# Kernel optimization log

Hardware: AMD Instinct MI355X
Metric: run time of the kernel (lower is better)

The kernel has to match this reference:

```python
import jax, jax.numpy as jnp
import numpy as np

B, T, V, E, H, C, L = 32, 120, 32000, 256, 512, 20, 10
LN_EPS = 1e-5

# static span enumeration matching the original loop order:
# for begin in range(T): for span_len in 1..L if begin+span_len-1 < T
_begs, _lens = [], []
for _b in range(T):
    for _l in range(1, min(L, T - _b) + 1):
        _begs.append(_b); _lens.append(_l)
BEGS = np.asarray(_begs, np.int32)   # [S], S = 1155
LENS = np.asarray(_lens, np.int32)
S = len(_begs)


def setup_inputs() -> dict:
    key = jax.random.key(0)
    ks = jax.random.split(key, 12)
    rn = lambda k, shape, s=0.05: (jax.random.normal(k, shape, jnp.float32) * s)
    return {
        "tokens": jax.random.randint(ks[0], (B, T), 0, V, dtype=jnp.int32),
        "emb": rn(ks[1], (V, E)),
        "w_ih_f": rn(ks[2], (4 * H, E)), "w_hh_f": rn(ks[3], (4 * H, H)),
        "b_ih_f": jnp.zeros((4 * H,), jnp.float32), "b_hh_f": jnp.zeros((4 * H,), jnp.float32),
        "w_ih_b": rn(ks[4], (4 * H, E)), "w_hh_b": rn(ks[5], (4 * H, H)),
        "b_ih_b": jnp.zeros((4 * H,), jnp.float32), "b_hh_b": jnp.zeros((4 * H,), jnp.float32),
        "lin1_w": rn(ks[6], (H, 2 * H)), "lin1_b": jnp.zeros((H,), jnp.float32),
        "lin2_w": rn(ks[7], (H, H)), "lin2_b": jnp.zeros((H,), jnp.float32),
        "ln_g": jnp.ones((H,), jnp.float32), "ln_b": jnp.zeros((H,), jnp.float32),
        "label_w": rn(ks[8], (H, C)), "label_b": rn(ks[9], (C,)),
    }


def _lstm_dir(x, w_ih, w_hh, b_ih, b_hh, reverse):
    # x: [B, T, E] -> hs: [B, T, H]; torch gate order i, f, g, o
    xs = jnp.swapaxes(x, 0, 1)          # [T, B, E]
    if reverse:
        xs = xs[::-1]
    xg = xs @ w_ih.T + (b_ih + b_hh)    # [T, B, 4H] input contribution precomputed
    h0 = jnp.zeros((x.shape[0], w_hh.shape[1]), x.dtype)

    def step(carry, g_in):
        h, c = carry
        g = g_in + h @ w_hh.T
        i, f, gg, o = jnp.split(g, 4, axis=-1)
        c = jax.nn.sigmoid(f) * c + jax.nn.sigmoid(i) * jnp.tanh(gg)
        h = jax.nn.sigmoid(o) * jnp.tanh(c)
        return (h, c), h

    _, hs = jax.lax.scan(step, (h0, h0), xg)
    if reverse:
        hs = hs[::-1]
    return jnp.swapaxes(hs, 0, 1)


def reference(tokens, emb, w_ih_f, w_hh_f, b_ih_f, b_hh_f,
              w_ih_b, w_hh_b, b_ih_b, b_hh_b,
              lin1_w, lin1_b, lin2_w, lin2_b, ln_g, ln_b,
              label_w, label_b):
    x = emb[tokens]                                          # [B, T, E]
    fwd = _lstm_dir(x, w_ih_f, w_hh_f, b_ih_f, b_hh_f, False)
    bwd = _lstm_dir(x, w_ih_b, w_hh_b, b_ih_b, b_hh_b, True)
    rnn_out = jnp.concatenate([fwd, bwd], axis=-1)           # [B, T, 2H]

    # non_linear: Linear -> Dropout(eval: identity) -> ReLU -> Linear -> LayerNorm
    h = jax.nn.relu(rnn_out @ lin1_w.T + lin1_b)
    h = h @ lin2_w.T + lin2_b
    mu = jnp.mean(h, axis=-1, keepdims=True)
    var = jnp.var(h, axis=-1, keepdims=True)
    token_repr = (h - mu) / jnp.sqrt(var + LN_EPS) * ln_g + ln_b  # [B, T, H]

    # span mean pooling via exclusive cumsum: mean over [beg, beg+len)
    cs = jnp.concatenate(
        [jnp.zeros_like(token_repr[:, :1]), jnp.cumsum(token_repr, axis=1)], axis=1)  # [B, T+1, H]
    begs = jnp.asarray(BEGS)
    ends = jnp.asarray(BEGS + LENS)
    inv_len = 1.0 / jnp.asarray(LENS, token_repr.dtype)[:, None]
    spans = (cs[:, ends] - cs[:, begs]) * inv_len            # [B, S, H]
    span_reprs = spans.reshape(-1, spans.shape[-1])          # [B*S, H], bid-major order

    score = jax.nn.log_softmax(span_reprs @ label_w + label_b, axis=0)
    return score
```

## Files before the change

kernel.cpp:

```cpp
#include <hip/hip_runtime.h>

#define B_ 32
#define T_ 120
#define E_ 256
#define H_ 512
#define NSPAN 36960

typedef __attribute__((ext_vector_type(8))) short short8;
typedef __attribute__((ext_vector_type(4))) short sshort4;
typedef __attribute__((ext_vector_type(4))) float f32x4;
typedef __attribute__((ext_vector_type(4))) unsigned int u32x4;
typedef unsigned long long ull;

__device__ __forceinline__ short f2bf(float x) {
    union { float f; unsigned u; } v; v.f = x;
    unsigned r = v.u + 0x7fffu + ((v.u >> 16) & 1u);
    return (short)(r >> 16);
}
__device__ __forceinline__ float bf2f(unsigned short x) {
    union { unsigned u; float f; } v; v.u = ((unsigned)x) << 16;
    return v.f;
}

#define LDC(dst, addr) \
    asm volatile("global_load_dwordx4 %0, %1, off sc0 sc1" : "=v"(dst) : "v"(addr))

__global__ void k_gather(const int* __restrict__ tokens, const float* __restrict__ emb,
                         short* __restrict__ xbf) {
    int m = blockIdx.x;
    int t = m >> 5, b = m & 31;
    int tok = tokens[b * T_ + t];
    int e = threadIdx.x;
    xbf[(size_t)m * E_ + e] = f2bf(emb[(size_t)tok * E_ + e]);
}

__global__ void k_convert(const float* __restrict__ src, short* __restrict__ dst, int n8) {
    int i = blockIdx.x * blockDim.x + threadIdx.x;
    if (i >= n8) return;
    const float4* s4 = (const float4*)src + (size_t)i * 2;
    float4 a = s4[0], b = s4[1];
    short8 o;
    o[0]=f2bf(a.x); o[1]=f2bf(a.y); o[2]=f2bf(a.z); o[3]=f2bf(a.w);
    o[4]=f2bf(b.x); o[5]=f2bf(b.y); o[6]=f2bf(b.z); o[7]=f2bf(b.w);
    *(short8*)(dst + (size_t)i * 8) = o;
}

__global__ void k_biascomb(const float* __restrict__ bf1, const float* __restrict__ bf2,
                           const float* __restrict__ bb1, const float* __restrict__ bb2,
                           float* __restrict__ out) {
    int i = blockIdx.x * 256 + threadIdx.x;
    out[i] = (i < 2048) ? (bf1[i] + bf2[i]) : (bb1[i - 2048] + bb2[i - 2048]);
}

template <int EPI>
__global__ void __launch_bounds__(256) k_gemm(const short* __restrict__ A,
                                              const short* __restrict__ W,
                                              const float* __restrict__ bias,
                                              float* __restrict__ outF,
                                              short* __restrict__ outB,
                                              int N, int K) {
    int w = threadIdx.x >> 6, l = threadIdx.x & 63;
    int la = l & 15, lb = l >> 4;
    int m0 = blockIdx.x * 64 + w * 16;
    int nb = blockIdx.y * 64;
    const short* Ap = A + (size_t)(m0 + la) * K + lb * 8;
    const short* Wp = W + (size_t)(nb + la) * K + lb * 8;
    f32x4 acc0 = {0.f,0.f,0.f,0.f}, acc1 = acc0, acc2 = acc0, acc3 = acc0;
    for (int k0 = 0; k0 < K; k0 += 32) {
        short8 a  = *(const short8*)(Ap + k0);
        short8 b0 = *(const short8*)(Wp + k0);
        short8 b1 = *(const short8*)(Wp + (size_t)16 * K + k0);
        short8 b2 = *(const short8*)(Wp + (size_t)32 * K + k0);
        short8 b3 = *(const short8*)(Wp + (size_t)48 * K + k0);
        acc0 = __builtin_amdgcn_mfma_f32_16x16x32_bf16(a, b0, acc0, 0, 0, 0);
        acc1 = __builtin_amdgcn_mfma_f32_16x16x32_bf16(a, b1, acc1, 0, 0, 0);
        acc2 = __builtin_amdgcn_mfma_f32_16x16x32_bf16(a, b2, acc2, 0, 0, 0);
        acc3 = __builtin_amdgcn_mfma_f32_16x16x32_bf16(a, b3, acc3, 0, 0, 0);
    }
    f32x4 accs[4] = {acc0, acc1, acc2, acc3};
    #pragma unroll
    for (int j = 0; j < 4; ++j) {
        int n = nb + j * 16 + la;
        float bv = bias[n];
        if (EPI == 2) {
            int mb = m0 + lb * 4;
            int t = mb >> 5, b0i = mb & 31;
            sshort4 pk;
            #pragma unroll
            for (int r = 0; r < 4; ++r) pk[r] = f2bf(accs[j][r] + bv);
            *(sshort4*)(outB + (((size_t)t * 4096 + n) << 5) + b0i) = pk;
        } else {
            #pragma unroll
            for (int r = 0; r < 4; ++r) {
                int m = m0 + lb * 4 + r;
                float v = accs[j][r] + bv;
                if (EPI == 0) outF[(size_t)m * N + n] = v;
                else          outB[(size_t)m * N + n] = f2bf(fmaxf(v, 0.f));
            }
        }
    }
}

__global__ void __launch_bounds__(256, 1) k_lstm(const short* __restrict__ xg,
                                                 const short* __restrict__ whh,
                                                 const short* __restrict__ hzero,
                                                 short* __restrict__ hsteps,
                                                 short* __restrict__ rnn) {
    __shared__ short wlds[4][16][512];
    __shared__ short hlds[32][512];
    __shared__ short hpack[4][32][4];
    int tid = threadIdx.x;
    int w = tid >> 6, l = tid & 63;
    int la = l & 15, lb = l >> 4;
    int bid = blockIdx.x;
    int dir = bid >> 5, jsl = bid & 31;
    int jw = jsl * 16 + w * 4;

    {
        char* base = (char*)&wlds[w][0][0];
        for (int cc = l; cc < 1024; cc += 64) {
            int rr = cc >> 6, c16 = cc & 63;
            int gate = rr >> 2, jj = rr & 3;
            short8 v = *(const short8*)(whh + ((size_t)dir * 2048 + gate * 512 + jw + jj) * 512 + c16 * 8);
            *(short8*)(base + rr * 1024 + ((c16 * 16) ^ ((rr & 7) << 4))) = v;
        }
    }
    __syncthreads();

    float cst[2][4] = {{0.f,0.f,0.f,0.f},{0.f,0.f,0.f,0.f}};
    int gate = la >> 2;
    int grow = dir * 2048 + gate * 512 + jw + (la & 3);
    const char* wrow = (const char*)&wlds[w][0][0] + la * 1024;
    const char* hrow0 = (const char*)&hlds[0][0] + la * 1024;
    const char* hrow1 = hrow0 + 16 * 1024;
    int swz = (la & 7) << 4;

    for (int s = 0; s < T_; ++s) {
        int t = dir ? (T_ - 1 - s) : s;
        const short* hb = (s == 0) ? hzero
                                   : (hsteps + ((size_t)(dir * T_ + (s - 1)) << 14));
        short* hn = hsteps + ((size_t)(dir * T_ + s) << 14);

        ull x0, x1;
        {
            u32x4 vv[8];
            const char* src = (const char*)hb;
            #pragma unroll
            for (int i = 0; i < 8; ++i)
                LDC(vv[i], src + (tid + 256 * i) * 16);
            const short* xgp = xg + ((size_t)t * 4096 + grow) * 32;
            x0 = *(const ull*)(xgp + lb * 4);
            x1 = *(const ull*)(xgp + 16 + lb * 4);
            asm volatile("s_waitcnt vmcnt(0)" ::: "memory");
            __builtin_amdgcn_sched_barrier(0);
            int tries = 0;
            while (true) {
                unsigned bad = 0;
                #pragma unroll
                for (int i = 0; i < 8; ++i)
                    if (vv[i][0] == 0xFFFFFFFFu || vv[i][2] == 0xFFFFFFFFu) bad |= 1u << i;
                if (!__any(bad != 0)) break;
                if (++tries > (1 << 17)) break;
                #pragma unroll
                for (int i = 0; i < 8; ++i)
                    if (bad & (1u << i)) LDC(vv[i], src + (tid + 256 * i) * 16);
                asm volatile("s_waitcnt vmcnt(0)" ::: "memory");
                __builtin_amdgcn_sched_barrier(0);
            }
            char* hdst = (char*)&hlds[0][0];
            #pragma unroll
            for (int i = 0; i < 8; ++i) {
                int byte = (tid + 256 * i) << 4;
                int row = byte >> 10, col = byte & 1023;
                *(u32x4*)(hdst + row * 1024 + (col ^ ((row & 7) << 4))) = vv[i];
            }
        }
        __syncthreads();

        float xv[2][4];
        #pragma unroll
        for (int r = 0; r < 4; ++r) {
            xv[0][r] = bf2f((unsigned short)((x0 >> (16 * r)) & 0xffffu));
            xv[1][r] = bf2f((unsigned short)((x1 >> (16 * r)) & 0xffffu));
        }

        f32x4 a0A = {0.f,0.f,0.f,0.f}, a0B = a0A, a1A = a0A, a1B = a0A;
        #pragma unroll
        for (int ks2 = 0; ks2 < 8; ++ks2) {
            int co0 = ((ks2 * 128) + lb * 16) ^ swz;
            int co1 = co0 ^ 64;
            short8 wA = *(const short8*)(wrow + co0);
            short8 wB = *(const short8*)(wrow + co1);
            short8 h0A = *(const short8*)(hrow0 + co0);
            short8 h0B = *(const short8*)(hrow0 + co1);
            short8 h1A = *(const short8*)(hrow1 + co0);
            short8 h1B = *(const short8*)(hrow1 + co1);
            a0A = __builtin_amdgcn_mfma_f32_16x16x32_bf16(h0A, wA, a0A, 0, 0, 0);
            a1A = __builtin_amdgcn_mfma_f32_16x16x32_bf16(h1A, wA, a1A, 0, 0, 0);
            a0B = __builtin_amdgcn_mfma_f32_16x16x32_bf16(h0B, wB, a0B, 0, 0, 0);
            a1B = __builtin_amdgcn_mfma_f32_16x16x32_bf16(h1B, wB, a1B, 0, 0, 0);
        }
        __syncthreads();
        f32x4 a0 = a0A + a0B, a1 = a1A + a1B;

        float val[2][4];
        #pragma unroll
        for (int mt = 0; mt < 2; ++mt) {
            #pragma unroll
            for (int r = 0; r < 4; ++r) {
                float x = (mt ? a1[r] : a0[r]) + xv[mt][r];
                val[mt][r] = (gate == 2) ? (1.f - 2.f / (1.f + __expf(2.f * x)))
                                         : (1.f / (1.f + __expf(-x)));
            }
        }

        #pragma unroll
        for (int mt = 0; mt < 2; ++mt) {
            #pragma unroll
            for (int r = 0; r < 4; ++r) {
                float v = val[mt][r];
                float vf = __shfl_xor(v, 4);
                float vg = __shfl_xor(v, 8);
                float vo = __shfl_xor(v, 12);
                if (la < 4) {
                    float c = vf * cst[mt][r] + v * vg;
                    cst[mt][r] = c;
                    float h = vo * (1.f - 2.f / (1.f + __expf(2.f * c)));
                    hpack[w][mt * 16 + lb * 4 + r][la] = f2bf(h);
                }
            }
        }
        asm volatile("s_waitcnt lgkmcnt(0)" ::: "memory");
        __builtin_amdgcn_sched_barrier(0);
        __builtin_amdgcn_wave_barrier();

        if (l < 32) {
            ull pk = *(const ull*)&hpack[w][l][0];
            short* hp = hn + (size_t)l * 512 + jw;
            asm volatile("global_store_dwordx2 %0, %1, off sc0 sc1" :: "v"(hp), "v"(pk) : "memory");
            *(ull*)(rnn + ((size_t)l * T_ + t) * 1024 + dir * 512 + jw) = pk;
        }
        __builtin_amdgcn_wave_barrier();
    }
}

__global__ void k_ln(const float* __restrict__ h2, const float* __restrict__ gam,
                     const float* __restrict__ bet, float* __restrict__ tr) {
    int w = threadIdx.x >> 6, l = threadIdx.x & 63;
    size_t row = (size_t)blockIdx.x * 4 + w;
    const float* x = h2 + row * 512;
    float v[8], s = 0.f, s2 = 0.f;
    #pragma unroll
    for (int i = 0; i < 8; ++i) { v[i] = x[l + 64 * i]; s += v[i]; s2 += v[i] * v[i]; }
    #pragma unroll
    for (int off = 32; off; off >>= 1) { s += __shfl_xor(s, off); s2 += __shfl_xor(s2, off); }
    float mu = s * (1.f / 512.f);
    float var = s2 * (1.f / 512.f) - mu * mu;
    float rstd = 1.f / sqrtf(var + 1e-5f);
    float* o = tr + row * 512;
    #pragma unroll
    for (int i = 0; i < 8; ++i) { int k = l + 64 * i; o[k] = (v[i] - mu) * rstd * gam[k] + bet[k]; }
}

__global__ void k_cumsum(const float* __restrict__ tr, float* __restrict__ cs) {
    int b = blockIdx.x, f = threadIdx.x;
    cs[((size_t)b * 121) * 512 + f] = 0.f;
    const float* src = tr + ((size_t)b * 120) * 512 + f;
    float* dst = cs + ((size_t)b * 121 + 1) * 512 + f;
    float run = 0.f;
    for (int t0 = 0; t0 < 120; t0 += 8) {
        float v[8];
        #pragma unroll
        for (int i = 0; i < 8; ++i) v[i] = src[(size_t)(t0 + i) * 512];
        #pragma unroll
        for (int i = 0; i < 8; ++i) { run += v[i]; dst[(size_t)(t0 + i) * 512] = run; }
    }
}

__global__ void __launch_bounds__(256) k_span(const float* __restrict__ cs,
                                              const float* __restrict__ lw,
                                              const float* __restrict__ lbias,
                                              float* __restrict__ out) {
    __shared__ float wl[20][512];
    for (int idx = threadIdx.x; idx < 20 * 512; idx += 256) {
        int c = idx >> 9, k = idx & 511;
        wl[c][k] = lw[(size_t)k * 20 + c];
    }
    __syncthreads();
    int w = threadIdx.x >> 6, l = threadIdx.x & 63;
    int nw = gridDim.x * 4;
    for (int sp = blockIdx.x * 4 + w; sp < NSPAN; sp += nw) {
        int b = sp / 1155, s = sp - b * 1155;
        int beg, len;
        if (s < 1110) { beg = s / 10; len = s - beg * 10 + 1; }
        else {
            int t2 = s - 1110; beg = 111; int ll = 9;
            while (t2 >= ll) { t2 -= ll; --ll; ++beg; }
            len = t2 + 1;
        }
        int end = beg + len;
        const float* ce = cs + ((size_t)b * 121 + end) * 512;
        const float* cb = cs + ((size_t)b * 121 + beg) * 512;
        float inv = 1.f / (float)len;
        float p[20];
        #pragma unroll
        for (int c = 0; c < 20; ++c) p[c] = 0.f;
        #pragma unroll
        for (int i = 0; i < 8; ++i) {
            int k = l + 64 * i;
            float d = (ce[k] - cb[k]) * inv;
            #pragma unroll
            for (int c = 0; c < 20; ++c) p[c] += d * wl[c][k];
        }
        #pragma unroll
        for (int off = 32; off; off >>= 1) {
            #pragma unroll
            for (int c = 0; c < 20; ++c) p[c] += __shfl_xor(p[c], off);
        }
        if (l == 0) {
            float* o = out + (size_t)sp * 20;
            #pragma unroll
            for (int c = 0; c < 20; ++c) o[c] = p[c] + lbias[c];
        }
    }
}

__global__ void __launch_bounds__(256) k_lsepart(const float* __restrict__ logits,
                                                 float2* __restrict__ part) {
    float m[20], sm[20];
    #pragma unroll
    for (int c = 0; c < 20; ++c) { m[c] = -1e30f; sm[c] = 0.f; }
    for (int row = blockIdx.x * 256 + threadIdx.x; row < NSPAN; row += gridDim.x * 256) {
        const float* r = logits + (size_t)row * 20;
        #pragma unroll
        for (int c = 0; c < 20; ++c) {
            float x = r[c];
            float nm = fmaxf(m[c], x);
            sm[c] = sm[c] * expf(m[c] - nm) + expf(x - nm);
            m[c] = nm;
        }
    }
    __shared__ float2 red[256][20];
    #pragma unroll
    for (int c = 0; c < 20; ++c) red[threadIdx.x][c] = make_float2(m[c], sm[c]);
    __syncthreads();
    for (int st = 128; st; st >>= 1) {
        if (threadIdx.x < st) {
            #pragma unroll
            for (int c = 0; c < 20; ++c) {
                float2 a = red[threadIdx.x][c], b = red[threadIdx.x + st][c];
                float nm = fmaxf(a.x, b.x);
                float ss = a.y * expf(a.x - nm) + b.y * expf(b.x - nm);
                red[threadIdx.x][c] = make_float2(nm, ss);
            }
        }
        __syncthreads();
    }
    if (threadIdx.x < 20) part[(size_t)blockIdx.x * 20 + threadIdx.x] = red[0][threadIdx.x];
}

__global__ void k_lsefin(const float2* __restrict__ part, int nparts, float* __restrict__ lse) {
    int c = threadIdx.x;
    if (c >= 20) return;
    float m = -1e30f, s = 0.f;
    for (int i = 0; i < nparts; ++i) {
        float2 a = part[(size_t)i * 20 + c];
        float nm = fmaxf(m, a.x);
        s = s * expf(m - nm) + a.y * expf(a.x - nm);
        m = nm;
    }
    lse[c] = m + logf(s);
}

__global__ void k_sub(float* __restrict__ out, const float* __restrict__ lse) {
    int i = blockIdx.x * 256 + threadIdx.x;
    if (i < NSPAN * 20) out[i] -= lse[i % 20];
}

extern "C" void kernel_launch(void* const* d_in, const int* in_sizes, int n_in,
                              void* d_out, int out_size, void* d_ws, size_t ws_size,
                              hipStream_t stream) {
    (void)in_sizes; (void)n_in; (void)out_size; (void)ws_size;
    const int*   tokens = (const int*)  d_in[0];
    const float* emb    = (const float*)d_in[1];
    const float* w_ih_f = (const float*)d_in[2];
    const float* w_hh_f = (const float*)d_in[3];
    const float* b_ih_f = (const float*)d_in[4];
    const float* b_hh_f = (const float*)d_in[5];
    const float* w_ih_b = (const float*)d_in[6];
    const float* w_hh_b = (const float*)d_in[7];
    const float* b_ih_b = (const float*)d_in[8];
    const float* b_hh_b = (const float*)d_in[9];
    const float* lin1_w = (const float*)d_in[10];
    const float* lin1_b = (const float*)d_in[11];
    const float* lin2_w = (const float*)d_in[12];
    const float* lin2_b = (const float*)d_in[13];
    const float* ln_g   = (const float*)d_in[14];
    const float* ln_b   = (const float*)d_in[15];
    const float* label_w= (const float*)d_in[16];
    const float* label_b= (const float*)d_in[17];
    float* out = (float*)d_out;

    char* ws = (char*)d_ws;
    size_t off = 0;
    auto alloc = [&](size_t bytes) { char* p = ws + off; off += (bytes + 255) & ~size_t(255); return p; };
    short*  xbf   = (short*)alloc(3840ull * 256 * 2);
    short*  wihbf = (short*)alloc(4096ull * 256 * 2);
    short*  whhbf = (short*)alloc(2ull * 2048 * 512 * 2);
    short*  l1wbf = (short*)alloc(512ull * 1024 * 2);
    short*  l2wbf = (short*)alloc(512ull * 512 * 2);
    float*  biasc = (float*)alloc(4096ull * 4);
    short*  xg    = (short*)alloc(120ull * 4096 * 32 * 2);
    short*  hzero = (short*)alloc(32ull * 512 * 2);
    short*  hsteps= (short*)alloc(2ull * 120 * 32 * 512 * 2);
    short*  rnn   = (short*)alloc(3840ull * 1024 * 2);
    float2* part  = (float2*)alloc(120ull * 20 * 8);
    float*  lse   = (float*)alloc(256);
    short*  h1    = (short*)whhbf;
    float*  h2    = (float*)hsteps;
    float*  tr    = (float*)xg;
    float*  cs    = (float*)((char*)xg + 8ull * 1024 * 1024);

    hipMemsetAsync(hzero, 0x00, 32ull * 512 * 2, stream);
    hipMemsetAsync(hsteps, 0xFF, 2ull * 120 * 32 * 512 * 2, stream);

    k_gather<<<3840, 256, 0, stream>>>(tokens, emb, xbf);
    int n8;
    n8 = 2048 * 256 / 8; k_convert<<<(n8 + 255) / 256, 256, 0, stream>>>(w_ih_f, wihbf, n8);
    n8 = 2048 * 256 / 8; k_convert<<<(n8 + 255) / 256, 256, 0, stream>>>(w_ih_b, wihbf + 2048ull * 256, n8);
    n8 = 2048 * 512 / 8; k_convert<<<(n8 + 255) / 256, 256, 0, stream>>>(w_hh_f, whhbf, n8);
    n8 = 2048 * 512 / 8; k_convert<<<(n8 + 255) / 256, 256, 0, stream>>>(w_hh_b, whhbf + 2048ull * 512, n8);
    n8 = 512 * 1024 / 8; k_convert<<<(n8 + 255) / 256, 256, 0, stream>>>(lin1_w, l1wbf, n8);
    n8 = 512 * 512 / 8;  k_convert<<<(n8 + 255) / 256, 256, 0, stream>>>(lin2_w, l2wbf, n8);
    k_biascomb<<<16, 256, 0, stream>>>(b_ih_f, b_hh_f, b_ih_b, b_hh_b, biasc);

    k_gemm<2><<<dim3(60, 64), 256, 0, stream>>>(xbf, wihbf, biasc, nullptr, xg, 4096, 256);
    k_lstm<<<64, 256, 0, stream>>>(xg, whhbf, hzero, hsteps, rnn);
    k_gemm<1><<<dim3(60, 8), 256, 0, stream>>>(rnn, l1wbf, lin1_b, nullptr, h1, 512, 1024);
    k_gemm<0><<<dim3(60, 8), 256, 0, stream>>>(h1, l2wbf, lin2_b, h2, nullptr, 512, 512);
    k_ln<<<960, 256, 0, stream>>>(h2, ln_g, ln_b, tr);
    k_cumsum<<<32, 512, 0, stream>>>(tr, cs);
    k_span<<<512, 256, 0, stream>>>(cs, label_w, label_b, out);
    k_lsepart<<<120, 256, 0, stream>>>(out, part);
    k_lsefin<<<1, 32, 0, stream>>>(part, 120, lse);
    k_sub<<<(NSPAN * 20 + 255) / 256, 256, 0, stream>>>(out, lse);
}
```

Baseline: 937.4 us.

## Keep LSTM weights in registers, add step counters, project before span pooling

After: 1.184 ms. 1.26x slower.

```diff
diff --git a/kernel.cpp b/kernel.cpp
--- a/kernel.cpp
+++ b/kernel.cpp
@@ -105,8 +105,8 @@
                                                  const short* __restrict__ whh,
                                                  const short* __restrict__ hzero,
                                                  short* __restrict__ hsteps,
-                                                 short* __restrict__ rnn) {
-    __shared__ short wlds[4][16][512];
+                                                 short* __restrict__ rnn,
+                                                 int* __restrict__ ctr) {
     __shared__ short hlds[32][512];
     __shared__ short hpack[4][32][4];
     int tid = threadIdx.x;
@@ -115,25 +115,22 @@
     int bid = blockIdx.x;
     int dir = bid >> 5, jsl = bid & 31;
     int jw = jsl * 16 + w * 4;
-
-    {
-        char* base = (char*)&wlds[w][0][0];
-        for (int cc = l; cc < 1024; cc += 64) {
-            int rr = cc >> 6, c16 = cc & 63;
-            int gate = rr >> 2, jj = rr & 3;
-            short8 v = *(const short8*)(whh + ((size_t)dir * 2048 + gate * 512 + jw + jj) * 512 + c16 * 8);
-            *(short8*)(base + rr * 1024 + ((c16 * 16) ^ ((rr & 7) << 4))) = v;
-        }
-    }
-    __syncthreads();
-
-    float cst[2][4] = {{0.f,0.f,0.f,0.f},{0.f,0.f,0.f,0.f}};
     int gate = la >> 2;
     int grow = dir * 2048 + gate * 512 + jw + (la & 3);
-    const char* wrow = (const char*)&wlds[w][0][0] + la * 1024;
+
+    short8 wf[16];
+    {
+        const short* wr = whh + (size_t)grow * 512 + lb * 8;
+        #pragma unroll
+        for (int ks = 0; ks < 16; ++ks) wf[ks] = *(const short8*)(wr + ks * 32);
+    }
+
     const char* hrow0 = (const char*)&hlds[0][0] + la * 1024;
     const char* hrow1 = hrow0 + 16 * 1024;
     int swz = (la & 7) << 4;
+    int* ctrd = ctr + dir * T_;
+
+    float cst[2][4] = {{0.f,0.f,0.f,0.f},{0.f,0.f,0.f,0.f}};
 
     for (int s = 0; s < T_; ++s) {
         int t = dir ? (T_ - 1 - s) : s;
@@ -143,14 +140,30 @@
 
         ull x0, x1;
         {
-            u32x4 vv[8];
-            const char* src = (const char*)hb;
-            #pragma unroll
-            for (int i = 0; i < 8; ++i)
-                LDC(vv[i], src + (tid + 256 * i) * 16);
             const short* xgp = xg + ((size_t)t * 4096 + grow) * 32;
             x0 = *(const ull*)(xgp + lb * 4);
             x1 = *(const ull*)(xgp + 16 + lb * 4);
+        }
+
+        if (s > 0) {
+            if (tid == 0) {
+                const int* cp = ctrd + (s - 1);
+                while (true) {
+                    int f;
+                    asm volatile("global_load_dword %0, %1, off sc0 sc1\n\ts_waitcnt vmcnt(0)"
+                                 : "=v"(f) : "v"(cp) : "memory");
+                    if (f >= 128) break;
+                }
+            }
+            __syncthreads();
+        }
+
+        {
+            u32x4 vv[8];
+            const char* src = (const char*)hb;
+            #pragma unroll
+            for (int i = 0; i < 8; ++i)
+                LDC(vv[i], src + (tid + 256 * i) * 16);
             asm volatile("s_waitcnt vmcnt(0)" ::: "memory");
             __builtin_amdgcn_sched_barrier(0);
             int tries = 0;
@@ -184,24 +197,21 @@
             xv[1][r] = bf2f((unsigned short)((x1 >> (16 * r)) & 0xffffu));
         }
 
-        f32x4 a0A = {0.f,0.f,0.f,0.f}, a0B = a0A, a1A = a0A, a1B = a0A;
-        #pragma unroll
-        for (int ks2 = 0; ks2 < 8; ++ks2) {
-            int co0 = ((ks2 * 128) + lb * 16) ^ swz;
-            int co1 = co0 ^ 64;
-            short8 wA = *(const short8*)(wrow + co0);
-            short8 wB = *(const short8*)(wrow + co1);
-            short8 h0A = *(const short8*)(hrow0 + co0);
-            short8 h0B = *(const short8*)(hrow0 + co1);
-            short8 h1A = *(const short8*)(hrow1 + co0);
-            short8 h1B = *(const short8*)(hrow1 + co1);
-            a0A = __builtin_amdgcn_mfma_f32_16x16x32_bf16(h0A, wA, a0A, 0, 0, 0);
-            a1A = __builtin_amdgcn_mfma_f32_16x16x32_bf16(h1A, wA, a1A, 0, 0, 0);
-            a0B = __builtin_amdgcn_mfma_f32_16x16x32_bf16(h0B, wB, a0B, 0, 0, 0);
-            a1B = __builtin_amdgcn_mfma_f32_16x16x32_bf16(h1B, wB, a1B, 0, 0, 0);
-        }
-        __syncthreads();
-        f32x4 a0 = a0A + a0B, a1 = a1A + a1B;
+        f32x4 ae0 = {0.f,0.f,0.f,0.f}, ao0 = ae0, ae1 = ae0, ao1 = ae0;
+        #pragma unroll
+        for (int ks = 0; ks < 16; ++ks) {
+            int co = (ks * 64 + lb * 16) ^ swz;
+            short8 h0 = *(const short8*)(hrow0 + co);
+            short8 h1 = *(const short8*)(hrow1 + co);
+            if (ks & 1) {
+                ao0 = __builtin_amdgcn_mfma_f32_16x16x32_bf16(h0, wf[ks], ao0, 0, 0, 0);
+                ao1 = __builtin_amdgcn_mfma_f32_16x16x32_bf16(h1, wf[ks], ao1, 0, 0, 0);
+            } else {
+                ae0 = __builtin_amdgcn_mfma_f32_16x16x32_bf16(h0, wf[ks], ae0, 0, 0, 0);
+                ae1 = __builtin_amdgcn_mfma_f32_16x16x32_bf16(h1, wf[ks], ae1, 0, 0, 0);
+            }
+        }
+        f32x4 a0 = ae0 + ao0, a1 = ae1 + ao1;
 
         float val[2][4];
         #pragma unroll
@@ -240,12 +250,23 @@
             asm volatile("global_store_dwordx2 %0, %1, off sc0 sc1" :: "v"(hp), "v"(pk) : "memory");
             *(ull*)(rnn + ((size_t)l * T_ + t) * 1024 + dir * 512 + jw) = pk;
         }
-        __builtin_amdgcn_wave_barrier();
-    }
-}
-
-__global__ void k_ln(const float* __restrict__ h2, const float* __restrict__ gam,
-                     const float* __restrict__ bet, float* __restrict__ tr) {
+        asm volatile("s_waitcnt vmcnt(0)" ::: "memory");
+        if (l == 0)
+            __hip_atomic_fetch_add(ctrd + s, 1, __ATOMIC_RELAXED, __HIP_MEMORY_SCOPE_AGENT);
+    }
+}
+
+__global__ void __launch_bounds__(256) k_lnproj(const float* __restrict__ h2,
+                                                const float* __restrict__ gam,
+                                                const float* __restrict__ bet,
+                                                const float* __restrict__ lw,
+                                                float* __restrict__ cs20raw) {
+    __shared__ float wl[20][512];
+    for (int idx = threadIdx.x; idx < 20 * 512; idx += 256) {
+        int c = idx >> 9, k = idx & 511;
+        wl[c][k] = lw[(size_t)k * 20 + c];
+    }
+    __syncthreads();
     int w = threadIdx.x >> 6, l = threadIdx.x & 63;
     size_t row = (size_t)blockIdx.x * 4 + w;
     const float* x = h2 + row * 512;
@@ -257,72 +278,61 @@
     float mu = s * (1.f / 512.f);
     float var = s2 * (1.f / 512.f) - mu * mu;
     float rstd = 1.f / sqrtf(var + 1e-5f);
-    float* o = tr + row * 512;
-    #pragma unroll
-    for (int i = 0; i < 8; ++i) { int k = l + 64 * i; o[k] = (v[i] - mu) * rstd * gam[k] + bet[k]; }
-}
-
-__global__ void k_cumsum(const float* __restrict__ tr, float* __restrict__ cs) {
-    int b = blockIdx.x, f = threadIdx.x;
-    cs[((size_t)b * 121) * 512 + f] = 0.f;
-    const float* src = tr + ((size_t)b * 120) * 512 + f;
-    float* dst = cs + ((size_t)b * 121 + 1) * 512 + f;
+    float p[20];
+    #pragma unroll
+    for (int c = 0; c < 20; ++c) p[c] = 0.f;
+    #pragma unroll
+    for (int i = 0; i < 8; ++i) {
+        int k = l + 64 * i;
+        float tr = (v[i] - mu) * rstd * gam[k] + bet[k];
+        #pragma unroll
+        for (int c = 0; c < 20; ++c) p[c] += tr * wl[c][k];
+    }
+    #pragma unroll
+    for (int off = 32; off; off >>= 1) {
+        #pragma unroll
+        for (int c = 0; c < 20; ++c) p[c] += __shfl_xor(p[c], off);
+    }
+    if (l == 0) {
+        float* o = cs20raw + row * 20;
+        #pragma unroll
+        for (int c = 0; c < 20; ++c) o[c] = p[c];
+    }
+}
+
+__global__ void k_cumsum20(const float* __restrict__ raw, float* __restrict__ cs20) {
+    int gid = blockIdx.x * 128 + threadIdx.x;
+    if (gid >= 640) return;
+    int b = gid / 20, c = gid - b * 20;
+    cs20[((size_t)b * 121) * 20 + c] = 0.f;
+    const float* src = raw + ((size_t)b * 120) * 20 + c;
+    float* dst = cs20 + ((size_t)b * 121 + 1) * 20 + c;
     float run = 0.f;
     for (int t0 = 0; t0 < 120; t0 += 8) {
         float v[8];
         #pragma unroll
-        for (int i = 0; i < 8; ++i) v[i] = src[(size_t)(t0 + i) * 512];
-        #pragma unroll
-        for (int i = 0; i < 8; ++i) { run += v[i]; dst[(size_t)(t0 + i) * 512] = run; }
-    }
-}
-
-__global__ void __launch_bounds__(256) k_span(const float* __restrict__ cs,
-                                              const float* __restrict__ lw,
-                                              const float* __restrict__ lbias,
-                                              float* __restrict__ out) {
-    __shared__ float wl[20][512];
-    for (int idx = threadIdx.x; idx < 20 * 512; idx += 256) {
-        int c = idx >> 9, k = idx & 511;
-        wl[c][k] = lw[(size_t)k * 20 + c];
-    }
-    __syncthreads();
-    int w = threadIdx.x >> 6, l = threadIdx.x & 63;
-    int nw = gridDim.x * 4;
-    for (int sp = blockIdx.x * 4 + w; sp < NSPAN; sp += nw) {
-        int b = sp / 1155, s = sp - b * 1155;
-        int beg, len;
-        if (s < 1110) { beg = s / 10; len = s - beg * 10 + 1; }
-        else {
-            int t2 = s - 1110; beg = 111; int ll = 9;
-            while (t2 >= ll) { t2 -= ll; --ll; ++beg; }
-            len = t2 + 1;
-        }
-        int end = beg + len;
-        const float* ce = cs + ((size_t)b * 121 + end) * 512;
-        const float* cb = cs + ((size_t)b * 121 + beg) * 512;
-        float inv = 1.f / (float)len;
-        float p[20];
-        #pragma unroll
-        for (int c = 0; c < 20; ++c) p[c] = 0.f;
-        #pragma unroll
-        for (int i = 0; i < 8; ++i) {
-            int k = l + 64 * i;
-            float d = (ce[k] - cb[k]) * inv;
-            #pragma unroll
-            for (int c = 0; c < 20; ++c) p[c] += d * wl[c][k];
-        }
-        #pragma unroll
-        for (int off = 32; off; off >>= 1) {
-            #pragma unroll
-            for (int c = 0; c < 20; ++c) p[c] += __shfl_xor(p[c], off);
-        }
-        if (l == 0) {
-            float* o = out + (size_t)sp * 20;
-            #pragma unroll
-            for (int c = 0; c < 20; ++c) o[c] = p[c] + lbias[c];
-        }
-    }
+        for (int i = 0; i < 8; ++i) v[i] = src[(size_t)(t0 + i) * 20];
+        #pragma unroll
+        for (int i = 0; i < 8; ++i) { run += v[i]; dst[(size_t)(t0 + i) * 20] = run; }
+    }
+}
+
+__global__ void k_span2(const float* __restrict__ cs20, const float* __restrict__ lbias,
+                        float* __restrict__ out) {
+    int i = blockIdx.x * 256 + threadIdx.x;
+    if (i >= NSPAN * 20) return;
+    int sp = i / 20, c = i - sp * 20;
+    int b = sp / 1155, s = sp - b * 1155;
+    int beg, len;
+    if (s < 1110) { beg = s / 10; len = s - beg * 10 + 1; }
+    else {
+        int t2 = s - 1110; beg = 111; int ll = 9;
+        while (t2 >= ll) { t2 -= ll; --ll; ++beg; }
+        len = t2 + 1;
+    }
+    int end = beg + len;
+    float d = cs20[((size_t)b * 121 + end) * 20 + c] - cs20[((size_t)b * 121 + beg) * 20 + c];
+    out[i] = d * (1.f / (float)len) + lbias[c];
 }
 
 __global__ void __launch_bounds__(256) k_lsepart(const float* __restrict__ logits,
@@ -404,25 +414,27 @@
     char* ws = (char*)d_ws;
     size_t off = 0;
     auto alloc = [&](size_t bytes) { char* p = ws + off; off += (bytes + 255) & ~size_t(255); return p; };
-    short*  xbf   = (short*)alloc(3840ull * 256 * 2);
-    short*  wihbf = (short*)alloc(4096ull * 256 * 2);
-    short*  whhbf = (short*)alloc(2ull * 2048 * 512 * 2);
-    short*  l1wbf = (short*)alloc(512ull * 1024 * 2);
-    short*  l2wbf = (short*)alloc(512ull * 512 * 2);
-    float*  biasc = (float*)alloc(4096ull * 4);
-    short*  xg    = (short*)alloc(120ull * 4096 * 32 * 2);
-    short*  hzero = (short*)alloc(32ull * 512 * 2);
-    short*  hsteps= (short*)alloc(2ull * 120 * 32 * 512 * 2);
-    short*  rnn   = (short*)alloc(3840ull * 1024 * 2);
-    float2* part  = (float2*)alloc(120ull * 20 * 8);
-    float*  lse   = (float*)alloc(256);
-    short*  h1    = (short*)whhbf;
-    float*  h2    = (float*)hsteps;
-    float*  tr    = (float*)xg;
-    float*  cs    = (float*)((char*)xg + 8ull * 1024 * 1024);
+    short*  xbf    = (short*)alloc(3840ull * 256 * 2);
+    short*  wihbf  = (short*)alloc(4096ull * 256 * 2);
+    short*  whhbf  = (short*)alloc(2ull * 2048 * 512 * 2);
+    short*  l1wbf  = (short*)alloc(512ull * 1024 * 2);
+    short*  l2wbf  = (short*)alloc(512ull * 512 * 2);
+    float*  biasc  = (float*)alloc(4096ull * 4);
+    short*  xg     = (short*)alloc(120ull * 4096 * 32 * 2);
+    short*  hzero  = (short*)alloc(32ull * 512 * 2);
+    short*  hsteps = (short*)alloc(2ull * 120 * 32 * 512 * 2);
+    short*  rnn    = (short*)alloc(3840ull * 1024 * 2);
+    int*    ctr    = (int*)  alloc(2ull * 120 * 4);
+    float*  cs20raw= (float*)alloc(3840ull * 20 * 4);
+    float*  cs20   = (float*)alloc(32ull * 121 * 20 * 4);
+    float2* part   = (float2*)alloc(120ull * 20 * 8);
+    float*  lse    = (float*)alloc(256);
+    short*  h1     = (short*)whhbf;
+    float*  h2     = (float*)hsteps;
 
     hipMemsetAsync(hzero, 0x00, 32ull * 512 * 2, stream);
     hipMemsetAsync(hsteps, 0xFF, 2ull * 120 * 32 * 512 * 2, stream);
+    hipMemsetAsync(ctr, 0x00, 2ull * 120 * 4, stream);
 
     k_gather<<<3840, 256, 0, stream>>>(tokens, emb, xbf);
     int n8;
@@ -435,12 +447,12 @@
     k_biascomb<<<16, 256, 0, stream>>>(b_ih_f, b_hh_f, b_ih_b, b_hh_b, biasc);
 
     k_gemm<2><<<dim3(60, 64), 256, 0, stream>>>(xbf, wihbf, biasc, nullptr, xg, 4096, 256);
-    k_lstm<<<64, 256, 0, stream>>>(xg, whhbf, hzero, hsteps, rnn);
+    k_lstm<<<64, 256, 0, stream>>>(xg, whhbf, hzero, hsteps, rnn, ctr);
     k_gemm<1><<<dim3(60, 8), 256, 0, stream>>>(rnn, l1wbf, lin1_b, nullptr, h1, 512, 1024);
     k_gemm<0><<<dim3(60, 8), 256, 0, stream>>>(h1, l2wbf, lin2_b, h2, nullptr, 512, 512);
-    k_ln<<<960, 256, 0, stream>>>(h2, ln_g, ln_b, tr);
-    k_cumsum<<<32, 512, 0, stream>>>(tr, cs);
-    k_span<<<512, 256, 0, stream>>>(cs, label_w, label_b, out);
+    k_lnproj<<<960, 256, 0, stream>>>(h2, ln_g, ln_b, label_w, cs20raw);
+    k_cumsum20<<<8, 128, 0, stream>>>(cs20raw, cs20);
+    k_span2<<<(NSPAN * 20 + 255) / 256, 256, 0, stream>>>(cs20, label_b, out);
     k_lsepart<<<120, 256, 0, stream>>>(out, part);
     k_lsefin<<<1, 32, 0, stream>>>(part, 120, lse);
     k_sub<<<(NSPAN * 20 + 255) / 256, 256, 0, stream>>>(out, lse);
```
